# Optimization experiments

Hardware: AMD Instinct MI355X
Metric: run time of the kernel (lower is better)

Reference implementation:

```python
import jax, jax.numpy as jnp
import numpy as np

H_GRU = 32  # GRU hidden size fixed to 32 in the module


def setup_inputs() -> dict:
    key = jax.random.key(0)
    ks = jax.random.split(key, 12)
    B, C_in, H, W = 64, 64, 48, 160
    C_out = 64
    s_in = 1.0 / np.sqrt(C_in)
    s_h = 1.0 / np.sqrt(H_GRU)
    u = lambda k, shape: jax.random.uniform(k, shape, jnp.float32, -s_h, s_h)
    return {
        "x": jax.random.normal(ks[0], (B, C_in, H, W), jnp.float32),
        "conv_w": jax.random.normal(ks[1], (C_out, C_in), jnp.float32) * s_in,
        "conv_b": jax.random.normal(ks[2], (C_out,), jnp.float32) * s_in,
        "wih_f": u(ks[3], (3 * H_GRU, C_out)),
        "whh_f": u(ks[4], (3 * H_GRU, H_GRU)),
        "bih_f": u(ks[5], (3 * H_GRU,)),
        "bhh_f": u(ks[6], (3 * H_GRU,)),
        "wih_b": u(ks[7], (3 * H_GRU, C_out)),
        "whh_b": u(ks[8], (3 * H_GRU, H_GRU)),
        "bih_b": u(ks[9], (3 * H_GRU,)),
        "bhh_b": u(ks[10], (3 * H_GRU,)),
    }


def _gru_scan(pre, whh, bhh):
    # pre: [N, T, 3H] input-side gate pre-activations (already x@Wih^T + bih)
    N = pre.shape[0]

    def step(h, g):
        gh = h @ whh.T + bhh
        gi_r, gi_z, gi_n = jnp.split(g, 3, axis=-1)
        gh_r, gh_z, gh_n = jnp.split(gh, 3, axis=-1)
        r = jax.nn.sigmoid(gi_r + gh_r)
        z = jax.nn.sigmoid(gi_z + gh_z)
        n = jnp.tanh(gi_n + r * gh_n)
        h_new = (1.0 - z) * n + z * h
        return h_new, h_new

    h0 = jnp.zeros((N, H_GRU), pre.dtype)
    _, ys = jax.lax.scan(step, h0, jnp.swapaxes(pre, 0, 1))  # ys: [T, N, H]
    return jnp.swapaxes(ys, 0, 1)  # [N, T, H]


def reference(x, conv_w, conv_b, wih_f, whh_f, bih_f, bhh_f,
              wih_b, whh_b, bih_b, bhh_b):
    B, C_in, H, W = x.shape
    # 1x1 conv fused with the NCHW->NHWC permute
    y = jnp.einsum('bchw,oc->bhwo', x, conv_w) + conv_b  # [B, H, W, C_out]
    C_out = y.shape[-1]
    seq = y.reshape(B * H, W, C_out)  # GRU batch = B*H, seq_len = W
    # forward direction
    pre_f = jnp.einsum('ntc,gc->ntg', seq, wih_f) + bih_f
    out_f = _gru_scan(pre_f, whh_f, bhh_f)
    # backward direction: scan reversed sequence, then flip output back
    seq_r = seq[:, ::-1, :]
    pre_b = jnp.einsum('ntc,gc->ntg', seq_r, wih_b) + bih_b
    out_b = _gru_scan(pre_b, whh_b, bhh_b)[:, ::-1, :]
    out = jnp.concatenate([out_f, out_b], axis=-1)  # [B*H, W, 2*H_GRU]
    out = out.reshape(B, H, W, 2 * H_GRU)
    return jnp.transpose(out, (0, 3, 1, 2))  # back to NCHW
```

## Files before the change

### kernel.cpp

```cpp
#include <hip/hip_runtime.h>


typedef _Float16 f16x8 __attribute__((ext_vector_type(8)));
typedef __fp16   pk16  __attribute__((ext_vector_type(2)));
typedef float f32x4 __attribute__((ext_vector_type(4)));

#define HWSTRIDE 7680
#define NCHUNK 10
#define WS_BIAS_OFF 24576

__global__ void fold_weights(const float* __restrict__ conv_w,
                             const float* __restrict__ conv_b,
                             const float* __restrict__ wih_f,
                             const float* __restrict__ bih_f,
                             const float* __restrict__ bhh_f,
                             const float* __restrict__ wih_b,
                             const float* __restrict__ bih_b,
                             const float* __restrict__ bhh_b,
                             void* wsv)
{
    _Float16* W2 = (_Float16*)wsv;
    float* bias = (float*)((char*)wsv + WS_BIAS_OFF);
    const int idx = blockIdx.x * 256 + threadIdx.x;
    if (idx < 12288) {
        const int d = idx / 6144, r = idx % 6144, g = r / 64, c = r % 64;
        const float* wih = d ? wih_b : wih_f;
        float acc = 0.f;
        for (int o = 0; o < 64; ++o) acc += wih[g * 64 + o] * conv_w[o * 64 + c];
        W2[idx] = (_Float16)acc;
    } else if (idx < 12288 + 256) {
        const int e = idx - 12288;
        const int d = e >> 7, rr = e & 127, kind = rr >> 5, j = rr & 31;
        const float* wih = d ? wih_b : wih_f;
        const float* bih = d ? bih_b : bih_f;
        const float* bhh = d ? bhh_b : bhh_f;
        float v;
        if (kind == 0 || kind == 1) {
            const int g = j + kind * 32;
            float b2 = bih[g];
            for (int o = 0; o < 64; ++o) b2 += wih[g * 64 + o] * conv_b[o];
            v = b2 + bhh[g];
        } else if (kind == 2) {
            const int g = j + 64;
            float b2 = bih[g];
            for (int o = 0; o < 64; ++o) b2 += wih[g * 64 + o] * conv_b[o];
            v = b2;
        } else {
            v = bhh[j + 64];
        }
        bias[(d * 4 + kind) * 32 + j] = v;
    }
}

__global__ __launch_bounds__(64, 3)
void gru_fused4(const float* __restrict__ x,
                const float* __restrict__ whh_f,
                const float* __restrict__ whh_b,
                const void* __restrict__ wsv,
                float* __restrict__ out)
{
    __shared__ __align__(16) _Float16 xt[64][18];
    __shared__ __align__(16) _Float16 s_pre[16][104];
    __shared__ __align__(16) float s_h[32];

    const int d    = blockIdx.x & 1;
    const int n    = blockIdx.x >> 1;
    const int b    = n / 48;
    const int h    = n % 48;
    const int lane = threadIdx.x;
    const int kh   = lane >> 5;
    const int j    = lane & 31;
    const int t16  = lane & 15;
    const int g8   = (lane >> 4) * 8;
    const int sc   = lane >> 2;
    const int stq  = lane & 3;

    const float* xbase = x + (size_t)b * (64 * HWSTRIDE) + (size_t)h * 160;

    const _Float16* W2 = (const _Float16*)wsv + (size_t)d * 96 * 64;
    f16x8 A[6][2];
    #pragma unroll
    for (int gt = 0; gt < 6; ++gt)
        #pragma unroll
        for (int kt = 0; kt < 2; ++kt)
            A[gt][kt] = *(const f16x8*)&W2[(gt * 16 + t16) * 64 + kt * 32 + g8];

    const float* whh = d ? whh_b : whh_f;
    float w[48];
    #pragma unroll
    for (int g = 0; g < 3; ++g)
        #pragma unroll
        for (int q = 0; q < 4; ++q) {
            const float4 wv = *(const float4*)&whh[(j + 32 * g) * 32 + kh * 16 + q * 4];
            w[g * 16 + q * 4 + 0] = wv.x; w[g * 16 + q * 4 + 1] = wv.y;
            w[g * 16 + q * 4 + 2] = wv.z; w[g * 16 + q * 4 + 3] = wv.w;
        }
    const float* bias = (const float*)((const char*)wsv + WS_BIAS_OFF);
    const float bc_r = bias[(d * 4 + 0) * 32 + j];
    const float bc_z = bias[(d * 4 + 1) * 32 + j];
    const float b2n  = bias[(d * 4 + 2) * 32 + j];
    const float bhn  = bias[(d * 4 + 3) * 32 + j];

    float* orow = out + (((size_t)b * 64 + (size_t)(d * 32 + j)) * 48 + h) * 160;

    float4 pf[4];
    auto issue_pf = [&](int cc) {
        const int w0 = d ? (144 - cc * 16) : (cc * 16);
        #pragma unroll
        for (int k = 0; k < 4; ++k)
            pf[k] = *(const float4*)(xbase + (size_t)(sc + 16 * k) * HWSTRIDE + w0 + stq * 4);
    };
    auto write_xt = [&]() {
        #pragma unroll
        for (int k = 0; k < 4; ++k) {
            pk16 lo = __builtin_amdgcn_cvt_pkrtz(pf[k].x, pf[k].y);
            pk16 hi = __builtin_amdgcn_cvt_pkrtz(pf[k].z, pf[k].w);
            *(pk16*)&xt[sc + 16 * k][stq * 4]     = lo;
            *(pk16*)&xt[sc + 16 * k][stq * 4 + 2] = hi;
        }
    };
    auto project = [&]() {
        f16x8 bf0, bf1;
        #pragma unroll
        for (int e = 0; e < 8; ++e) {
            bf0[e] = xt[g8 + e][t16];
            bf1[e] = xt[32 + g8 + e][t16];
        }
        const int row = d ? (15 - t16) : t16;
        #pragma unroll
        for (int gt = 0; gt < 6; ++gt) {
            f32x4 acc = {0.f, 0.f, 0.f, 0.f};
            acc = __builtin_amdgcn_mfma_f32_16x16x32_f16(A[gt][0], bf0, acc, 0, 0, 0);
            acc = __builtin_amdgcn_mfma_f32_16x16x32_f16(A[gt][1], bf1, acc, 0, 0, 0);
            pk16 o0 = __builtin_amdgcn_cvt_pkrtz(acc[0], acc[1]);
            pk16 o1 = __builtin_amdgcn_cvt_pkrtz(acc[2], acc[3]);
            *(pk16*)&s_pre[row][gt * 16 + (lane >> 4) * 4]     = o0;
            *(pk16*)&s_pre[row][gt * 16 + (lane >> 4) * 4 + 2] = o1;
        }
    };

    issue_pf(0);
    write_xt();
    issue_pf(1);
    project();
    if (kh == 0) s_h[j] = 0.f;
    float hcur = 0.f;

    for (int ci = 0; ci < NCHUNK; ++ci) {
        float hh[8];
        #pragma unroll
        for (int s = 0; s < 16; ++s) {
            const float pr = (float)s_pre[s][j];
            const float pz = (float)s_pre[s][j + 32];
            const float pn = (float)s_pre[s][j + 64];
            float4 h4[4];
            #pragma unroll
            for (int q = 0; q < 4; ++q) h4[q] = ((const float4*)&s_h[16 * kh])[q];
            const float* hv = (const float*)h4;
            float ar0 = 0.f, az0 = 0.f, an0 = 0.f;
            float ar1 = 0.f, az1 = 0.f, an1 = 0.f;
            #pragma unroll
            for (int k = 0; k < 16; k += 2) {
                const float h0 = hv[k], h1 = hv[k + 1];
                ar0 = fmaf(w[k],          h0, ar0);
                az0 = fmaf(w[16 + k],     h0, az0);
                an0 = fmaf(w[32 + k],     h0, an0);
                ar1 = fmaf(w[k + 1],      h1, ar1);
                az1 = fmaf(w[17 + k],     h1, az1);
                an1 = fmaf(w[33 + k],     h1, an1);
            }
            float ar = ar0 + ar1, az = az0 + az1, an = an0 + an1;
            ar += __shfl_xor(ar, 32);
            az += __shfl_xor(az, 32);
            an += __shfl_xor(an, 32);
            const float gr = ar + pr + bc_r;
            const float gz = az + pz + bc_z;
            const float r = __builtin_amdgcn_rcpf(1.f + __expf(-gr));
            const float z = __builtin_amdgcn_rcpf(1.f + __expf(-gz));
            float ta = (pn + b2n) + r * (an + bhn);
            ta = fminf(fmaxf(ta, -15.f), 15.f);
            const float e2 = __expf(2.f * ta);
            const float nn = (e2 - 1.f) * __builtin_amdgcn_rcpf(e2 + 1.f);
            hcur = (1.f - z) * nn + z * hcur;
            if (kh == 0) s_h[j] = hcur;
            asm volatile("" ::: "memory");
            if ((s >> 3) == kh) hh[s & 7] = hcur;
        }
        if (d == 0) {
            *(float4*)&orow[ci * 16 + 8 * kh] =
                make_float4(hh[0], hh[1], hh[2], hh[3]);
            *(float4*)&orow[ci * 16 + 8 * kh + 4] =
                make_float4(hh[4], hh[5], hh[6], hh[7]);
        } else {
            *(float4*)&orow[156 - ci * 16 - 8 * kh] =
                make_float4(hh[3], hh[2], hh[1], hh[0]);
            *(float4*)&orow[152 - ci * 16 - 8 * kh] =
                make_float4(hh[7], hh[6], hh[5], hh[4]);
        }
        if (ci < NCHUNK - 1) {
            write_xt();
            if (ci < NCHUNK - 2) issue_pf(ci + 2);
            project();
        }
    }
}

extern "C" void kernel_launch(void* const* d_in, const int* in_sizes, int n_in,
                              void* d_out, int out_size, void* d_ws, size_t ws_size,
                              hipStream_t stream) {
    (void)in_sizes; (void)n_in; (void)ws_size; (void)out_size;
    fold_weights<<<dim3(49), dim3(256), 0, stream>>>(
        (const float*)d_in[1],
        (const float*)d_in[2],
        (const float*)d_in[3],
        (const float*)d_in[5],
        (const float*)d_in[6],
        (const float*)d_in[7],
        (const float*)d_in[9],
        (const float*)d_in[10],
        d_ws);
    gru_fused4<<<dim3(6144), dim3(64), 0, stream>>>(
        (const float*)d_in[0],
        (const float*)d_in[4],
        (const float*)d_in[8],
        d_ws,
        (float*)d_out);
}
```

Before: 188.7 us.

## Batch 16 GRU rows per wave and compute recurrent matmul with MFMA

Each 64-lane block now processes 16 sequences (rows h) of one direction together, so the hidden-state recurrence h@Whh^T becomes a 16x96x32 MFMA per timestep instead of per-lane scalar FMAs with cross-half shuffles. The hidden state is stored in fp16 in a small LDS ring buffer, biases are folded into MFMA accumulators, and input projection runs in 4-step chunks with double-buffered staging. The grid drops from 6144 to 384 blocks, which cuts the total number of serial recurrence chains but leaves many CUs idle and relies on low-precision hidden-state feedback, which could accumulate error.

```diff
diff --git a/kernel.cpp b/kernel.cpp
--- a/kernel.cpp
+++ b/kernel.cpp
@@ -2,11 +2,12 @@
 
 
 typedef _Float16 f16x8 __attribute__((ext_vector_type(8)));
+typedef _Float16 f16x4 __attribute__((ext_vector_type(4)));
 typedef __fp16   pk16  __attribute__((ext_vector_type(2)));
-typedef float f32x4 __attribute__((ext_vector_type(4)));
+typedef float    f32x4 __attribute__((ext_vector_type(4)));
 
 #define HWSTRIDE 7680
-#define NCHUNK 10
+#define NCH 40
 #define WS_BIAS_OFF 24576
 
 __global__ void fold_weights(const float* __restrict__ conv_w,
@@ -52,155 +53,196 @@
     }
 }
 
-__global__ __launch_bounds__(64, 3)
-void gru_fused4(const float* __restrict__ x,
+static __device__ __forceinline__ unsigned pkh(float a, float b) {
+    pk16 p = __builtin_amdgcn_cvt_pkrtz(a, b);
+    return __builtin_bit_cast(unsigned, p);
+}
+
+__global__ __launch_bounds__(64, 1)
+void gru_fused5(const float* __restrict__ x,
                 const float* __restrict__ whh_f,
                 const float* __restrict__ whh_b,
                 const void* __restrict__ wsv,
                 float* __restrict__ out)
 {
-    __shared__ __align__(16) _Float16 xt[64][18];
-    __shared__ __align__(16) _Float16 s_pre[16][104];
-    __shared__ __align__(16) float s_h[32];
-
-    const int d    = blockIdx.x & 1;
-    const int n    = blockIdx.x >> 1;
-    const int b    = n / 48;
-    const int h    = n % 48;
-    const int lane = threadIdx.x;
-    const int kh   = lane >> 5;
-    const int j    = lane & 31;
-    const int t16  = lane & 15;
-    const int g8   = (lane >> 4) * 8;
-    const int sc   = lane >> 2;
-    const int stq  = lane & 3;
-
-    const float* xbase = x + (size_t)b * (64 * HWSTRIDE) + (size_t)h * 160;
+    __shared__ _Float16 x_lds[2][64][17][4];
+    __shared__ _Float16 s_pre[2][4][16][104];
+    __shared__ _Float16 hring[4][16][40];
+
+    const int d     = blockIdx.x & 1;
+    const int group = blockIdx.x >> 1;
+    const int b     = group / 3;
+    const int h0    = (group % 3) * 16;
+    const int lane  = threadIdx.x;
+    const int q     = lane >> 4;
+    const int s16   = lane & 15;
+
+    const float* xb = x + (size_t)b * 64 * HWSTRIDE + (size_t)h0 * 160;
 
     const _Float16* W2 = (const _Float16*)wsv + (size_t)d * 96 * 64;
-    f16x8 A[6][2];
+    f16x8 W2A[6][2];
     #pragma unroll
     for (int gt = 0; gt < 6; ++gt)
         #pragma unroll
         for (int kt = 0; kt < 2; ++kt)
-            A[gt][kt] = *(const f16x8*)&W2[(gt * 16 + t16) * 64 + kt * 32 + g8];
+            W2A[gt][kt] = *(const f16x8*)&W2[(gt * 16 + s16) * 64 + kt * 32 + q * 8];
 
     const float* whh = d ? whh_b : whh_f;
-    float w[48];
-    #pragma unroll
-    for (int g = 0; g < 3; ++g)
-        #pragma unroll
-        for (int q = 0; q < 4; ++q) {
-            const float4 wv = *(const float4*)&whh[(j + 32 * g) * 32 + kh * 16 + q * 4];
-            w[g * 16 + q * 4 + 0] = wv.x; w[g * 16 + q * 4 + 1] = wv.y;
-            w[g * 16 + q * 4 + 2] = wv.z; w[g * 16 + q * 4 + 3] = wv.w;
-        }
-    const float* bias = (const float*)((const char*)wsv + WS_BIAS_OFF);
-    const float bc_r = bias[(d * 4 + 0) * 32 + j];
-    const float bc_z = bias[(d * 4 + 1) * 32 + j];
-    const float b2n  = bias[(d * 4 + 2) * 32 + j];
-    const float bhn  = bias[(d * 4 + 3) * 32 + j];
-
-    float* orow = out + (((size_t)b * 64 + (size_t)(d * 32 + j)) * 48 + h) * 160;
-
-    float4 pf[4];
-    auto issue_pf = [&](int cc) {
-        const int w0 = d ? (144 - cc * 16) : (cc * 16);
-        #pragma unroll
-        for (int k = 0; k < 4; ++k)
-            pf[k] = *(const float4*)(xbase + (size_t)(sc + 16 * k) * HWSTRIDE + w0 + stq * 4);
+    f16x8 whhA[6];
+    #pragma unroll
+    for (int gt = 0; gt < 6; ++gt)
+        #pragma unroll
+        for (int e = 0; e < 8; ++e)
+            whhA[gt][e] = (_Float16)whh[(gt * 16 + s16) * 32 + q * 8 + e];
+
+    const float* bias = (const float*)((const char*)wsv + WS_BIAS_OFF) + d * 128;
+    float biasC[6][4];
+    #pragma unroll
+    for (int r = 0; r < 4; ++r) {
+        biasC[0][r] = bias[      4 * q + r];
+        biasC[1][r] = bias[ 16 + 4 * q + r];
+        biasC[2][r] = bias[ 32 + 4 * q + r];
+        biasC[3][r] = bias[ 48 + 4 * q + r];
+        biasC[4][r] = bias[ 64 + 4 * q + r];
+        biasC[5][r] = bias[ 80 + 4 * q + r];
+    }
+    float bhN[2][4];
+    #pragma unroll
+    for (int r = 0; r < 4; ++r) {
+        bhN[0][r] = bias[ 96 + 4 * q + r];
+        bhN[1][r] = bias[112 + 4 * q + r];
+    }
+
+    float4 pf[16];
+    auto stage_issue = [&](int cn) {
+        const int w0 = d ? (156 - cn * 4) : (cn * 4);
+        const float* base = xb + s16 * 160 + w0;
+        #pragma unroll
+        for (int i = 0; i < 16; ++i)
+            pf[i] = *(const float4*)(base + (size_t)(i * 4 + q) * HWSTRIDE);
     };
-    auto write_xt = [&]() {
-        #pragma unroll
-        for (int k = 0; k < 4; ++k) {
-            pk16 lo = __builtin_amdgcn_cvt_pkrtz(pf[k].x, pf[k].y);
-            pk16 hi = __builtin_amdgcn_cvt_pkrtz(pf[k].z, pf[k].w);
-            *(pk16*)&xt[sc + 16 * k][stq * 4]     = lo;
-            *(pk16*)&xt[sc + 16 * k][stq * 4 + 2] = hi;
+    auto stage_write = [&](int buf) {
+        #pragma unroll
+        for (int i = 0; i < 16; ++i) {
+            const int c = i * 4 + q;
+            uint2 v;
+            if (d == 0) { v.x = pkh(pf[i].x, pf[i].y); v.y = pkh(pf[i].z, pf[i].w); }
+            else        { v.x = pkh(pf[i].w, pf[i].z); v.y = pkh(pf[i].y, pf[i].x); }
+            *(uint2*)&x_lds[buf][c][s16][0] = v;
         }
     };
-    auto project = [&]() {
-        f16x8 bf0, bf1;
-        #pragma unroll
-        for (int e = 0; e < 8; ++e) {
-            bf0[e] = xt[g8 + e][t16];
-            bf1[e] = xt[32 + g8 + e][t16];
-        }
-        const int row = d ? (15 - t16) : t16;
-        #pragma unroll
-        for (int gt = 0; gt < 6; ++gt) {
-            f32x4 acc = {0.f, 0.f, 0.f, 0.f};
-            acc = __builtin_amdgcn_mfma_f32_16x16x32_f16(A[gt][0], bf0, acc, 0, 0, 0);
-            acc = __builtin_amdgcn_mfma_f32_16x16x32_f16(A[gt][1], bf1, acc, 0, 0, 0);
-            pk16 o0 = __builtin_amdgcn_cvt_pkrtz(acc[0], acc[1]);
-            pk16 o1 = __builtin_amdgcn_cvt_pkrtz(acc[2], acc[3]);
-            *(pk16*)&s_pre[row][gt * 16 + (lane >> 4) * 4]     = o0;
-            *(pk16*)&s_pre[row][gt * 16 + (lane >> 4) * 4 + 2] = o1;
+    auto project = [&](int buf) {
+        #pragma unroll
+        for (int tt = 0; tt < 4; ++tt) {
+            f16x8 B0, B1;
+            #pragma unroll
+            for (int e = 0; e < 8; ++e) {
+                B0[e] = x_lds[buf][     q * 8 + e][s16][tt];
+                B1[e] = x_lds[buf][32 + q * 8 + e][s16][tt];
+            }
+            #pragma unroll
+            for (int gt = 0; gt < 6; ++gt) {
+                f32x4 acc = {biasC[gt][0], biasC[gt][1], biasC[gt][2], biasC[gt][3]};
+                acc = __builtin_amdgcn_mfma_f32_16x16x32_f16(W2A[gt][0], B0, acc, 0, 0, 0);
+                acc = __builtin_amdgcn_mfma_f32_16x16x32_f16(W2A[gt][1], B1, acc, 0, 0, 0);
+                uint2 v; v.x = pkh(acc[0], acc[1]); v.y = pkh(acc[2], acc[3]);
+                *(uint2*)&s_pre[buf][tt][s16][gt * 16 + 4 * q] = v;
+            }
         }
     };
 
-    issue_pf(0);
-    write_xt();
-    issue_pf(1);
-    project();
-    if (kh == 0) s_h[j] = 0.f;
-    float hcur = 0.f;
-
-    for (int ci = 0; ci < NCHUNK; ++ci) {
-        float hh[8];
-        #pragma unroll
-        for (int s = 0; s < 16; ++s) {
-            const float pr = (float)s_pre[s][j];
-            const float pz = (float)s_pre[s][j + 32];
-            const float pn = (float)s_pre[s][j + 64];
-            float4 h4[4];
-            #pragma unroll
-            for (int q = 0; q < 4; ++q) h4[q] = ((const float4*)&s_h[16 * kh])[q];
-            const float* hv = (const float*)h4;
-            float ar0 = 0.f, az0 = 0.f, an0 = 0.f;
-            float ar1 = 0.f, az1 = 0.f, an1 = 0.f;
-            #pragma unroll
-            for (int k = 0; k < 16; k += 2) {
-                const float h0 = hv[k], h1 = hv[k + 1];
-                ar0 = fmaf(w[k],          h0, ar0);
-                az0 = fmaf(w[16 + k],     h0, az0);
-                an0 = fmaf(w[32 + k],     h0, an0);
-                ar1 = fmaf(w[k + 1],      h1, ar1);
-                az1 = fmaf(w[17 + k],     h1, az1);
-                an1 = fmaf(w[33 + k],     h1, an1);
-            }
-            float ar = ar0 + ar1, az = az0 + az1, an = an0 + an1;
-            ar += __shfl_xor(ar, 32);
-            az += __shfl_xor(az, 32);
-            an += __shfl_xor(an, 32);
-            const float gr = ar + pr + bc_r;
-            const float gz = az + pz + bc_z;
-            const float r = __builtin_amdgcn_rcpf(1.f + __expf(-gr));
-            const float z = __builtin_amdgcn_rcpf(1.f + __expf(-gz));
-            float ta = (pn + b2n) + r * (an + bhn);
-            ta = fminf(fmaxf(ta, -15.f), 15.f);
-            const float e2 = __expf(2.f * ta);
-            const float nn = (e2 - 1.f) * __builtin_amdgcn_rcpf(e2 + 1.f);
-            hcur = (1.f - z) * nn + z * hcur;
-            if (kh == 0) s_h[j] = hcur;
-            asm volatile("" ::: "memory");
-            if ((s >> 3) == kh) hh[s & 7] = hcur;
-        }
-        if (d == 0) {
-            *(float4*)&orow[ci * 16 + 8 * kh] =
-                make_float4(hh[0], hh[1], hh[2], hh[3]);
-            *(float4*)&orow[ci * 16 + 8 * kh + 4] =
-                make_float4(hh[4], hh[5], hh[6], hh[7]);
-        } else {
-            *(float4*)&orow[156 - ci * 16 - 8 * kh] =
-                make_float4(hh[3], hh[2], hh[1], hh[0]);
-            *(float4*)&orow[152 - ci * 16 - 8 * kh] =
-                make_float4(hh[7], hh[6], hh[5], hh[4]);
-        }
-        if (ci < NCHUNK - 1) {
-            write_xt();
-            if (ci < NCHUNK - 2) issue_pf(ci + 2);
-            project();
+    float hprev[8];
+    #pragma unroll
+    for (int u = 0; u < 8; ++u) hprev[u] = 0.f;
+
+    stage_issue(0);
+    stage_write(0);
+    project(0);
+
+    auto gate = [](float v) { return __builtin_amdgcn_rcpf(1.f + __expf(-v)); };
+
+    #pragma unroll 1
+    for (int ci = 0; ci < NCH; ++ci) {
+        const int buf = ci & 1;
+        if (ci < NCH - 1) stage_issue(ci + 1);
+
+        #pragma unroll
+        for (int tt = 0; tt < 4; ++tt) {
+            const int t = ci * 4 + tt;
+            const _Float16* pr = &s_pre[buf][tt][s16][0];
+            f16x4 p0 = *(const f16x4*)&pr[      4 * q];
+            f16x4 p1 = *(const f16x4*)&pr[ 16 + 4 * q];
+            f16x4 p2 = *(const f16x4*)&pr[ 32 + 4 * q];
+            f16x4 p3 = *(const f16x4*)&pr[ 48 + 4 * q];
+            f16x4 p4 = *(const f16x4*)&pr[ 64 + 4 * q];
+            f16x4 p5 = *(const f16x4*)&pr[ 80 + 4 * q];
+            f16x8 hB = {};
+            if (t > 0) hB = *(const f16x8*)&hring[(t - 1) & 3][s16][8 * q];
+
+            f32x4 aR0 = {(float)p0[0], (float)p0[1], (float)p0[2], (float)p0[3]};
+            f32x4 aR1 = {(float)p1[0], (float)p1[1], (float)p1[2], (float)p1[3]};
+            f32x4 aZ0 = {(float)p2[0], (float)p2[1], (float)p2[2], (float)p2[3]};
+            f32x4 aZ1 = {(float)p3[0], (float)p3[1], (float)p3[2], (float)p3[3]};
+            f32x4 aN0 = {bhN[0][0], bhN[0][1], bhN[0][2], bhN[0][3]};
+            f32x4 aN1 = {bhN[1][0], bhN[1][1], bhN[1][2], bhN[1][3]};
+            aR0 = __builtin_amdgcn_mfma_f32_16x16x32_f16(whhA[0], hB, aR0, 0, 0, 0);
+            aR1 = __builtin_amdgcn_mfma_f32_16x16x32_f16(whhA[1], hB, aR1, 0, 0, 0);
+            aZ0 = __builtin_amdgcn_mfma_f32_16x16x32_f16(whhA[2], hB, aZ0, 0, 0, 0);
+            aZ1 = __builtin_amdgcn_mfma_f32_16x16x32_f16(whhA[3], hB, aZ1, 0, 0, 0);
+            aN0 = __builtin_amdgcn_mfma_f32_16x16x32_f16(whhA[4], hB, aN0, 0, 0, 0);
+            aN1 = __builtin_amdgcn_mfma_f32_16x16x32_f16(whhA[5], hB, aN1, 0, 0, 0);
+
+            float hnew[8];
+            #pragma unroll
+            for (int r = 0; r < 4; ++r) {
+                const float rr = gate(aR0[r]);
+                const float zz = gate(aZ0[r]);
+                float ta = fmaf(rr, aN0[r], (float)p4[r]);
+                ta = fminf(fmaxf(ta, -15.f), 15.f);
+                const float e2 = __expf(2.f * ta);
+                const float nn = (e2 - 1.f) * __builtin_amdgcn_rcpf(e2 + 1.f);
+                hnew[r] = (1.f - zz) * nn + zz * hprev[r];
+            }
+            #pragma unroll
+            for (int r = 0; r < 4; ++r) {
+                const float rr = gate(aR1[r]);
+                const float zz = gate(aZ1[r]);
+                float ta = fmaf(rr, aN1[r], (float)p5[r]);
+                ta = fminf(fmaxf(ta, -15.f), 15.f);
+                const float e2 = __expf(2.f * ta);
+                const float nn = (e2 - 1.f) * __builtin_amdgcn_rcpf(e2 + 1.f);
+                hnew[4 + r] = (1.f - zz) * nn + zz * hprev[4 + r];
+            }
+            uint2 w0; w0.x = pkh(hnew[0], hnew[1]); w0.y = pkh(hnew[2], hnew[3]);
+            uint2 w1; w1.x = pkh(hnew[4], hnew[5]); w1.y = pkh(hnew[6], hnew[7]);
+            *(uint2*)&hring[t & 3][s16][     4 * q] = w0;
+            *(uint2*)&hring[t & 3][s16][16 + 4 * q] = w1;
+            #pragma unroll
+            for (int u = 0; u < 8; ++u) hprev[u] = hnew[u];
+        }
+
+        {
+            const int jj = lane >> 1;
+            const int sb = (lane & 1) * 8;
+            float* obase = out + (size_t)b * 491520 + (size_t)(d * 32 + jj) * 7680;
+            const int wb = d ? (156 - ci * 4) : (ci * 4);
+            #pragma unroll
+            for (int p = 0; p < 8; ++p) {
+                const int s = sb + p;
+                float4 v;
+                if (d == 0)
+                    v = make_float4((float)hring[0][s][jj], (float)hring[1][s][jj],
+                                    (float)hring[2][s][jj], (float)hring[3][s][jj]);
+                else
+                    v = make_float4((float)hring[3][s][jj], (float)hring[2][s][jj],
+                                    (float)hring[1][s][jj], (float)hring[0][s][jj]);
+                *(float4*)&obase[(h0 + s) * 160 + wb] = v;
+            }
+        }
+
+        if (ci < NCH - 1) {
+            stage_write(buf ^ 1);
+            project(buf ^ 1);
         }
     }
 }
@@ -219,7 +261,7 @@
         (const float*)d_in[9],
         (const float*)d_in[10],
         d_ws);
-    gru_fused4<<<dim3(6144), dim3(64), 0, stream>>>(
+    gru_fused5<<<dim3(384), dim3(64), 0, stream>>>(
         (const float*)d_in[0],
         (const float*)d_in[4],
         (const float*)d_in[8],
```

Result: slower. 374.6 us (+98.5%).
